# Performance work log

Measured on AMD Instinct MI355X. Metric: run time of the kernel, lower is better.

## Reference

```python
import jax, jax.numpy as jnp
import numpy as np

N, D_IN, D_H, K, E = 100000, 128, 256, 16, 3200000


def setup_inputs() -> dict:
    key = jax.random.key(0)
    ks = jax.random.split(key, 6)
    x = jax.random.normal(ks[0], (N, D_IN), dtype=jnp.float32)
    edge_index = jax.random.randint(ks[1], (2, E), 0, N, dtype=jnp.int64)
    # Linear params (stored as [in, out] for x @ W + b)
    W1 = jax.random.normal(ks[2], (D_IN, D_H), dtype=jnp.float32) * 0.05
    b1 = jnp.zeros((D_H,), dtype=jnp.float32)
    W2 = jax.random.normal(ks[3], (D_H, K), dtype=jnp.float32) * 0.05
    b2 = jnp.zeros((K,), dtype=jnp.float32)
    return {"x": x, "edge_index": edge_index, "W1": W1, "b1": b1, "W2": W2, "b2": b2}


def reference(x, edge_index, W1, b1, W2, b2):
    # 2-layer MLP + row softmax -> soft cluster assignments C [N, K]
    h = jax.nn.relu(x @ W1 + b1)
    C = jax.nn.softmax(h @ W2 + b2, axis=1)
    # trace((C C^T)^T @ adj) == sum over edges (u,v) of C[u] . C[v]
    # (exact, incl. duplicate edges, since to_dense_adj scatter-adds 1 per edge)
    src, dst = edge_index[0], edge_index[1]
    edge_sum = jnp.sum(C[src] * C[dst])  # [E, K] gathered dot products, reduced
    num_edges = jnp.asarray(edge_index.shape[1], dtype=C.dtype)  # adj.sum()
    modularity_loss = -edge_sum / num_edges
    return (C, modularity_loss)
```

## Files before the change

### kernel.cpp

```cpp
#include <hip/hip_runtime.h>

#define N_NODES 100000
#define D_INF   128
#define D_HID   256
#define K_CL    16
#define N_TILES (N_NODES / 16)
#define N_EDGES 3200000
#define EDGE_BLOCKS (N_EDGES / 1024)

typedef __attribute__((ext_vector_type(8))) __bf16  bf16x8;
typedef __attribute__((ext_vector_type(8))) unsigned short u16x8;
typedef __attribute__((ext_vector_type(4))) float   f32x4;

__device__ __forceinline__ unsigned short f2bf(float f) {
    unsigned int u = __builtin_bit_cast(unsigned int, f);
    u += 0x7fffu + ((u >> 16) & 1u);
    return (unsigned short)(u >> 16);
}
__device__ __forceinline__ float bflo(unsigned int p) {
    return __builtin_bit_cast(float, p << 16);
}
__device__ __forceinline__ float bfhi(unsigned int p) {
    return __builtin_bit_cast(float, p & 0xffff0000u);
}

__global__ void prep_kernel(const float* __restrict__ W1,
                            const float* __restrict__ W2,
                            unsigned short* __restrict__ w1t,
                            unsigned short* __restrict__ w2t)
{
    const int i = blockIdx.x * 256 + threadIdx.x;
    if (i < D_INF * D_HID) {
        const int n = i >> 7, k = i & 127;
        w1t[i] = f2bf(W1[k * D_HID + n]);
    }
    if (i < D_HID * K_CL) {
        const int t = i >> 8, n = i & 255;
        w2t[i] = f2bf(W2[n * K_CL + t]);
    }
}

#define W1S 136
#define CHS 40

__global__ __launch_bounds__(256, 2) void mlp_kernel(
    const float* __restrict__ x, const unsigned short* __restrict__ W1T,
    const float* __restrict__ b1, const unsigned short* __restrict__ W2T,
    const float* __restrict__ b2, float* __restrict__ C,
    unsigned short* __restrict__ Cb)
{
    __shared__ unsigned short w1s[256 * W1S];
    __shared__ unsigned short chbuf[4][2][16 * CHS];
    __shared__ float b1s[D_HID];

    const int tid  = threadIdx.x;
    const int wv   = tid >> 6;
    const int lane = tid & 63;
    const int c    = lane & 15;
    const int q    = lane >> 4;

    #pragma unroll
    for (int it = 0; it < 16; ++it) {
        const int idx = it * 256 + tid;
        const int row = idx >> 4, ch = idx & 15;
        const uint4 v = ((const uint4*)W1T)[idx];
        *(uint4*)&w1s[row * W1S + ch * 8] = v;
    }
    if (tid < D_HID) b1s[tid] = b1[tid];

    bf16x8 w2f[8];
    #pragma unroll
    for (int kc2 = 0; kc2 < 8; ++kc2)
        w2f[kc2] = *(const bf16x8*)(W2T + (size_t)c * D_HID + kc2 * 32 + q * 8);
    const float b2v = b2[c];
    __syncthreads();

    unsigned short* const chA = &chbuf[wv][0][0];
    unsigned short* const chB = &chbuf[wv][1][0];

    const int wid     = blockIdx.x * 4 + wv;
    const int wstride = gridDim.x * 4;

    for (int tile = wid; tile < N_TILES; tile += wstride) {
        const int m0 = tile * 16;

        const float* xrow = x + (size_t)(m0 + c) * D_INF + q * 8;
        bf16x8 afr[4];
        #pragma unroll
        for (int kc = 0; kc < 4; ++kc) {
            const float4 xa = *(const float4*)(xrow + kc * 32);
            const float4 xb = *(const float4*)(xrow + kc * 32 + 4);
            u16x8 af;
            af[0] = f2bf(xa.x); af[1] = f2bf(xa.y); af[2] = f2bf(xa.z); af[3] = f2bf(xa.w);
            af[4] = f2bf(xb.x); af[5] = f2bf(xb.y); af[6] = f2bf(xb.z); af[7] = f2bf(xb.w);
            afr[kc] = __builtin_bit_cast(bf16x8, af);
        }

        f32x4 acc2 = (f32x4){0.f, 0.f, 0.f, 0.f};
        #pragma unroll
        for (int kc2 = 0; kc2 < 8; ++kc2) {
            unsigned short* const wbuf = (kc2 & 1) ? chB : chA;

            float ph[2][4];
            #pragma unroll
            for (int half = 0; half < 2; ++half) {
                const int nt = kc2 * 2 + half;
                f32x4 a1 = (f32x4){0.f, 0.f, 0.f, 0.f};
                #pragma unroll
                for (int kc = 0; kc < 4; ++kc) {
                    const bf16x8 bf =
                        *(const bf16x8*)&w1s[(nt * 16 + c) * W1S + kc * 32 + q * 8];
                    a1 = __builtin_amdgcn_mfma_f32_16x16x32_bf16(afr[kc], bf, a1, 0, 0, 0);
                }
                const float bv = b1s[nt * 16 + c];
                #pragma unroll
                for (int r = 0; r < 4; ++r)
                    ph[half][r] = fmaxf(a1[r] + bv, 0.f);
            }

            if (kc2 > 0) {
                unsigned short* const rbuf = (kc2 & 1) ? chA : chB;
                const bf16x8 a2 = *(const bf16x8*)&rbuf[c * CHS + q * 8];
                acc2 = __builtin_amdgcn_mfma_f32_16x16x32_bf16(a2, w2f[kc2 - 1], acc2, 0, 0, 0);
            }

            #pragma unroll
            for (int half = 0; half < 2; ++half)
                #pragma unroll
                for (int r = 0; r < 4; ++r)
                    wbuf[(4 * q + r) * CHS + half * 16 + c] = f2bf(ph[half][r]);
        }
        {
            const bf16x8 a2 = *(const bf16x8*)&chB[c * CHS + q * 8];
            acc2 = __builtin_amdgcn_mfma_f32_16x16x32_bf16(a2, w2f[7], acc2, 0, 0, 0);
        }

        #pragma unroll
        for (int r = 0; r < 4; ++r) {
            const float l = acc2[r] + b2v;
            float mx = l;
            mx = fmaxf(mx, __shfl_xor(mx, 1));
            mx = fmaxf(mx, __shfl_xor(mx, 2));
            mx = fmaxf(mx, __shfl_xor(mx, 4));
            mx = fmaxf(mx, __shfl_xor(mx, 8));
            const float e = __expf(l - mx);
            float sm = e;
            sm += __shfl_xor(sm, 1);
            sm += __shfl_xor(sm, 2);
            sm += __shfl_xor(sm, 4);
            sm += __shfl_xor(sm, 8);
            const float p = e / sm;
            const size_t o = (size_t)(m0 + 4 * q + r) * K_CL + c;
            C[o]  = p;
            Cb[o] = f2bf(p);
        }
    }
}

__global__ __launch_bounds__(256) void edge_kernel(
    const int* __restrict__ ei, const unsigned short* __restrict__ Cb,
    float* __restrict__ partials)
{
    __shared__ float red[4];
    const int tid  = threadIdx.x;
    const int lane = tid & 63;
    const int wv   = tid >> 6;
    const int base = (blockIdx.x * 4 + wv) * 256;

    int u[4], v[4];
    #pragma unroll
    for (int j = 0; j < 4; ++j) {
        u[j] = ei[base + j * 64 + lane];
        v[j] = ei[N_EDGES + base + j * 64 + lane];
    }

    const int half8 = (lane & 1) * 8;
    const int sl    = lane >> 1;

    float s = 0.f;
    #pragma unroll
    for (int g = 0; g < 8; ++g) {
        const int src = (g & 1) * 32 + sl;
        const int ue  = __shfl(u[g >> 1], src);
        const int ve  = __shfl(v[g >> 1], src);
        const uint4 a = *(const uint4*)(Cb + (size_t)ue * K_CL + half8);
        const uint4 b = *(const uint4*)(Cb + (size_t)ve * K_CL + half8);
        s = fmaf(bflo(a.x), bflo(b.x), s);
        s = fmaf(bfhi(a.x), bfhi(b.x), s);
        s = fmaf(bflo(a.y), bflo(b.y), s);
        s = fmaf(bfhi(a.y), bfhi(b.y), s);
        s = fmaf(bflo(a.z), bflo(b.z), s);
        s = fmaf(bfhi(a.z), bfhi(b.z), s);
        s = fmaf(bflo(a.w), bflo(b.w), s);
        s = fmaf(bfhi(a.w), bfhi(b.w), s);
    }
    s += __shfl_xor(s, 1);
    s += __shfl_xor(s, 2);
    s += __shfl_xor(s, 4);
    s += __shfl_xor(s, 8);
    s += __shfl_xor(s, 16);
    s += __shfl_xor(s, 32);
    if (lane == 0) red[wv] = s;
    __syncthreads();
    if (tid == 0) partials[blockIdx.x] = red[0] + red[1] + red[2] + red[3];
}

__global__ __launch_bounds__(256) void finalize_kernel(
    const float* __restrict__ partials, float* __restrict__ out)
{
    __shared__ float red[4];
    const int tid = threadIdx.x;
    float s = 0.f;
    for (int i = tid; i < EDGE_BLOCKS; i += 256) s += partials[i];
    s += __shfl_xor(s, 1);
    s += __shfl_xor(s, 2);
    s += __shfl_xor(s, 4);
    s += __shfl_xor(s, 8);
    s += __shfl_xor(s, 16);
    s += __shfl_xor(s, 32);
    if ((tid & 63) == 0) red[tid >> 6] = s;
    __syncthreads();
    if (tid == 0)
        out[(size_t)N_NODES * K_CL] =
            -(red[0] + red[1] + red[2] + red[3]) / (float)N_EDGES;
}

extern "C" void kernel_launch(void* const* d_in, const int* in_sizes, int n_in,
                              void* d_out, int out_size, void* d_ws, size_t ws_size,
                              hipStream_t stream) {
    const float* x  = (const float*)d_in[0];
    const int*   ei = (const int*)  d_in[1];
    const float* W1 = (const float*)d_in[2];
    const float* b1 = (const float*)d_in[3];
    const float* W2 = (const float*)d_in[4];
    const float* b2 = (const float*)d_in[5];
    float* out = (float*)d_out;

    unsigned short* w1t      = (unsigned short*)d_ws;
    unsigned short* w2t      = (unsigned short*)((char*)d_ws + 65536);
    unsigned short* Cb       = (unsigned short*)((char*)d_ws + 73760);
    float*          partials = (float*)((char*)d_ws + 3273760);

    prep_kernel<<<128, 256, 0, stream>>>(W1, W2, w1t, w2t);
    mlp_kernel<<<512, 256, 0, stream>>>(x, w1t, b1, w2t, b2, out, Cb);
    edge_kernel<<<EDGE_BLOCKS, 256, 0, stream>>>(ei, Cb, partials);
    finalize_kernel<<<1, 256, 0, stream>>>(partials, out);
}
```

Baseline: 156.1 us.

## Split hidden dimension across waves with W1 held in registers

Each block now processes one 16-row tile, and each of the four waves computes a quarter of the hidden units. The wave's W1 slice stays in registers, which removes the shared-memory copy of W1 and its LDS reads. The per-wave partial layer-2 logits are summed through a double-buffered shared buffer with one block barrier per tile, and each wave writes only its own rows. This frees LDS for higher occupancy (launch bounds 3, 768 blocks), at the cost of a per-tile __syncthreads and all four waves redundantly loading the same x rows.

```diff
diff --git a/kernel.cpp b/kernel.cpp
--- a/kernel.cpp
+++ b/kernel.cpp
@@ -40,18 +40,16 @@
     }
 }
 
-#define W1S 136
 #define CHS 40
 
-__global__ __launch_bounds__(256, 2) void mlp_kernel(
+__global__ __launch_bounds__(256, 3) void mlp_kernel(
     const float* __restrict__ x, const unsigned short* __restrict__ W1T,
     const float* __restrict__ b1, const unsigned short* __restrict__ W2T,
     const float* __restrict__ b2, float* __restrict__ C,
     unsigned short* __restrict__ Cb)
 {
-    __shared__ unsigned short w1s[256 * W1S];
-    __shared__ unsigned short chbuf[4][2][16 * CHS];
-    __shared__ float b1s[D_HID];
+    __shared__ unsigned short hbuf[4][2][16 * CHS];
+    __shared__ f32x4 pbuf[2][4][64];
 
     const int tid  = threadIdx.x;
     const int wv   = tid >> 6;
@@ -59,29 +57,28 @@
     const int c    = lane & 15;
     const int q    = lane >> 4;
 
-    #pragma unroll
-    for (int it = 0; it < 16; ++it) {
-        const int idx = it * 256 + tid;
-        const int row = idx >> 4, ch = idx & 15;
-        const uint4 v = ((const uint4*)W1T)[idx];
-        *(uint4*)&w1s[row * W1S + ch * 8] = v;
-    }
-    if (tid < D_HID) b1s[tid] = b1[tid];
-
-    bf16x8 w2f[8];
-    #pragma unroll
-    for (int kc2 = 0; kc2 < 8; ++kc2)
-        w2f[kc2] = *(const bf16x8*)(W2T + (size_t)c * D_HID + kc2 * 32 + q * 8);
+    bf16x8 bfr[4][4];
+    #pragma unroll
+    for (int i = 0; i < 4; ++i)
+        #pragma unroll
+        for (int kc = 0; kc < 4; ++kc)
+            bfr[i][kc] = *(const bf16x8*)(
+                W1T + (size_t)((4 * wv + i) * 16 + c) * D_INF + kc * 32 + q * 8);
+    bf16x8 w2f[2];
+    #pragma unroll
+    for (int j = 0; j < 2; ++j)
+        w2f[j] = *(const bf16x8*)(
+            W2T + (size_t)c * D_HID + (2 * wv + j) * 32 + q * 8);
+    float b1v[4];
+    #pragma unroll
+    for (int i = 0; i < 4; ++i) b1v[i] = b1[(4 * wv + i) * 16 + c];
     const float b2v = b2[c];
-    __syncthreads();
-
-    unsigned short* const chA = &chbuf[wv][0][0];
-    unsigned short* const chB = &chbuf[wv][1][0];
-
-    const int wid     = blockIdx.x * 4 + wv;
-    const int wstride = gridDim.x * 4;
-
-    for (int tile = wid; tile < N_TILES; tile += wstride) {
+
+    unsigned short* const ch0 = &hbuf[wv][0][0];
+    unsigned short* const ch1 = &hbuf[wv][1][0];
+
+    int p = 0;
+    for (int tile = blockIdx.x; tile < N_TILES; tile += gridDim.x) {
         const int m0 = tile * 16;
 
         const float* xrow = x + (size_t)(m0 + c) * D_INF + q * 8;
@@ -96,48 +93,41 @@
             afr[kc] = __builtin_bit_cast(bf16x8, af);
         }
 
+        #pragma unroll
+        for (int i = 0; i < 4; ++i) {
+            f32x4 a1 = (f32x4){0.f, 0.f, 0.f, 0.f};
+            #pragma unroll
+            for (int kc = 0; kc < 4; ++kc)
+                a1 = __builtin_amdgcn_mfma_f32_16x16x32_bf16(afr[kc], bfr[i][kc], a1, 0, 0, 0);
+            const float bv = b1v[i];
+            unsigned short* const cb = (i >> 1) ? ch1 : ch0;
+            const int colb = (i & 1) * 16 + c;
+            #pragma unroll
+            for (int r = 0; r < 4; ++r)
+                cb[(4 * q + r) * CHS + colb] = f2bf(fmaxf(a1[r] + bv, 0.f));
+        }
+
         f32x4 acc2 = (f32x4){0.f, 0.f, 0.f, 0.f};
-        #pragma unroll
-        for (int kc2 = 0; kc2 < 8; ++kc2) {
-            unsigned short* const wbuf = (kc2 & 1) ? chB : chA;
-
-            float ph[2][4];
-            #pragma unroll
-            for (int half = 0; half < 2; ++half) {
-                const int nt = kc2 * 2 + half;
-                f32x4 a1 = (f32x4){0.f, 0.f, 0.f, 0.f};
-                #pragma unroll
-                for (int kc = 0; kc < 4; ++kc) {
-                    const bf16x8 bf =
-                        *(const bf16x8*)&w1s[(nt * 16 + c) * W1S + kc * 32 + q * 8];
-                    a1 = __builtin_amdgcn_mfma_f32_16x16x32_bf16(afr[kc], bf, a1, 0, 0, 0);
-                }
-                const float bv = b1s[nt * 16 + c];
-                #pragma unroll
-                for (int r = 0; r < 4; ++r)
-                    ph[half][r] = fmaxf(a1[r] + bv, 0.f);
-            }
-
-            if (kc2 > 0) {
-                unsigned short* const rbuf = (kc2 & 1) ? chA : chB;
-                const bf16x8 a2 = *(const bf16x8*)&rbuf[c * CHS + q * 8];
-                acc2 = __builtin_amdgcn_mfma_f32_16x16x32_bf16(a2, w2f[kc2 - 1], acc2, 0, 0, 0);
-            }
-
-            #pragma unroll
-            for (int half = 0; half < 2; ++half)
-                #pragma unroll
-                for (int r = 0; r < 4; ++r)
-                    wbuf[(4 * q + r) * CHS + half * 16 + c] = f2bf(ph[half][r]);
-        }
         {
-            const bf16x8 a2 = *(const bf16x8*)&chB[c * CHS + q * 8];
-            acc2 = __builtin_amdgcn_mfma_f32_16x16x32_bf16(a2, w2f[7], acc2, 0, 0, 0);
-        }
+            const bf16x8 a20 = *(const bf16x8*)&ch0[c * CHS + q * 8];
+            acc2 = __builtin_amdgcn_mfma_f32_16x16x32_bf16(a20, w2f[0], acc2, 0, 0, 0);
+            const bf16x8 a21 = *(const bf16x8*)&ch1[c * CHS + q * 8];
+            acc2 = __builtin_amdgcn_mfma_f32_16x16x32_bf16(a21, w2f[1], acc2, 0, 0, 0);
+        }
+
+        pbuf[p][wv][lane] = acc2;
+        __syncthreads();
+        f32x4 lg = pbuf[p][0][lane];
+        #pragma unroll
+        for (int j = 1; j < 4; ++j) {
+            const f32x4 o = pbuf[p][j][lane];
+            lg[0] += o[0]; lg[1] += o[1]; lg[2] += o[2]; lg[3] += o[3];
+        }
+        p ^= 1;
 
         #pragma unroll
         for (int r = 0; r < 4; ++r) {
-            const float l = acc2[r] + b2v;
+            const float l = lg[r] + b2v;
             float mx = l;
             mx = fmaxf(mx, __shfl_xor(mx, 1));
             mx = fmaxf(mx, __shfl_xor(mx, 2));
@@ -149,10 +139,12 @@
             sm += __shfl_xor(sm, 2);
             sm += __shfl_xor(sm, 4);
             sm += __shfl_xor(sm, 8);
-            const float p = e / sm;
-            const size_t o = (size_t)(m0 + 4 * q + r) * K_CL + c;
-            C[o]  = p;
-            Cb[o] = f2bf(p);
+            if (q == wv) {
+                const float pr = e / sm;
+                const size_t o = (size_t)(m0 + 4 * q + r) * K_CL + c;
+                C[o]  = pr;
+                Cb[o] = f2bf(pr);
+            }
         }
     }
 }
@@ -242,7 +234,7 @@
     float*          partials = (float*)((char*)d_ws + 3273760);
 
     prep_kernel<<<128, 256, 0, stream>>>(W1, W2, w1t, w2t);
-    mlp_kernel<<<512, 256, 0, stream>>>(x, w1t, b1, w2t, b2, out, Cb);
+    mlp_kernel<<<768, 256, 0, stream>>>(x, w1t, b1, w2t, b2, out, Cb);
     edge_kernel<<<EDGE_BLOCKS, 256, 0, stream>>>(ei, Cb, partials);
     finalize_kernel<<<1, 256, 0, stream>>>(partials, out);
 }
```

Measured after the change: 176.6 us. 13.2% more time.
